# Kernel tuning notes

Measured on AMD Instinct MI355X. Metric: run time of the kernel, lower is better.

The kernel has to match this reference:

```python
import jax, jax.numpy as jnp
import numpy as np

B, S, T = 32, 400, 64
V, E, H = 32000, 256, 512


def _lstm_step(x, h, c, W_ih, W_hh, b):
    # PyTorch LSTM gate order: i, f, g, o
    g = x @ W_ih.T + h @ W_hh.T + b
    i, f, gg, o = jnp.split(g, 4, axis=-1)
    i = jax.nn.sigmoid(i)
    f = jax.nn.sigmoid(f)
    gg = jnp.tanh(gg)
    o = jax.nn.sigmoid(o)
    c_new = f * c + i * gg
    h_new = o * jnp.tanh(c_new)
    return h_new, c_new


def setup_inputs() -> dict:
    key = jax.random.key(0)
    ks = jax.random.split(key, 32)
    d = {}
    d['src'] = jax.random.randint(ks[0], (B, S), 1, V)
    d['src_lengths'] = jnp.full((B,), S, dtype=jnp.int32)
    d['tgt'] = jax.random.randint(ks[1], (B, T), 1, V)
    sc = 0.05
    emb = jax.random.normal(ks[2], (V, E), jnp.float32) * sc
    d['emb'] = emb.at[0].set(0.0)  # padding_idx=0
    d['enc_W_ih_f'] = jax.random.normal(ks[3], (4 * H, E), jnp.float32) * sc
    d['enc_W_hh_f'] = jax.random.normal(ks[4], (4 * H, H), jnp.float32) * sc
    d['enc_b_ih_f'] = jax.random.normal(ks[5], (4 * H,), jnp.float32) * sc
    d['enc_b_hh_f'] = jax.random.normal(ks[6], (4 * H,), jnp.float32) * sc
    d['enc_W_ih_b'] = jax.random.normal(ks[7], (4 * H, E), jnp.float32) * sc
    d['enc_W_hh_b'] = jax.random.normal(ks[8], (4 * H, H), jnp.float32) * sc
    d['enc_b_ih_b'] = jax.random.normal(ks[9], (4 * H,), jnp.float32) * sc
    d['enc_b_hh_b'] = jax.random.normal(ks[10], (4 * H,), jnp.float32) * sc
    d['enc_init_h'] = jax.random.uniform(ks[11], (2, H), jnp.float32, -0.01, 0.01)
    d['enc_init_c'] = jax.random.uniform(ks[12], (2, H), jnp.float32, -0.01, 0.01)
    d['dec_h_W'] = jax.random.normal(ks[13], (H, 2 * H), jnp.float32) * sc
    d['dec_c_W'] = jax.random.normal(ks[14], (H, 2 * H), jnp.float32) * sc
    d['cell_W_ih'] = jax.random.normal(ks[15], (4 * H, E), jnp.float32) * sc
    d['cell_W_hh'] = jax.random.normal(ks[16], (4 * H, H), jnp.float32) * sc
    d['cell_b_ih'] = jax.random.normal(ks[17], (4 * H,), jnp.float32) * sc
    d['cell_b_hh'] = jax.random.normal(ks[18], (4 * H,), jnp.float32) * sc
    d['attn_W'] = jax.random.normal(ks[19], (H, 2 * H), jnp.float32) * sc
    d['attn_b'] = jax.random.normal(ks[20], (H,), jnp.float32) * sc
    d['concat_W'] = jax.random.normal(ks[21], (H, 3 * H), jnp.float32) * sc
    d['concat_b'] = jax.random.normal(ks[22], (H,), jnp.float32) * sc
    d['out_W'] = jax.random.normal(ks[23], (V, H), jnp.float32) * sc
    d['out_b'] = jax.random.normal(ks[24], (V,), jnp.float32) * sc
    return d


def reference(src, src_lengths, tgt, emb,
              enc_W_ih_f, enc_W_hh_f, enc_b_ih_f, enc_b_hh_f,
              enc_W_ih_b, enc_W_hh_b, enc_b_ih_b, enc_b_hh_b,
              enc_init_h, enc_init_c, dec_h_W, dec_c_W,
              cell_W_ih, cell_W_hh, cell_b_ih, cell_b_hh,
              attn_W, attn_b, concat_W, concat_b, out_W, out_b):
    Bs, Ss = src.shape
    Hs = enc_init_h.shape[1]
    xe = emb[src].transpose(1, 0, 2)  # [S, B, E]

    # ---- bi-LSTM encoder (all lengths == S, so packing is identity) ----
    h0f = jnp.broadcast_to(enc_init_h[0], (Bs, Hs))
    c0f = jnp.broadcast_to(enc_init_c[0], (Bs, Hs))
    h0b = jnp.broadcast_to(enc_init_h[1], (Bs, Hs))
    c0b = jnp.broadcast_to(enc_init_c[1], (Bs, Hs))

    def enc_fwd(carry, x):
        h, c = carry
        h, c = _lstm_step(x, h, c, enc_W_ih_f, enc_W_hh_f, enc_b_ih_f + enc_b_hh_f)
        return (h, c), h

    def enc_bwd(carry, x):
        h, c = carry
        h, c = _lstm_step(x, h, c, enc_W_ih_b, enc_W_hh_b, enc_b_ih_b + enc_b_hh_b)
        return (h, c), h

    (hf, cf), out_f = jax.lax.scan(enc_fwd, (h0f, c0f), xe)
    (hb, cb), out_b_seq = jax.lax.scan(enc_bwd, (h0b, c0b), xe[::-1])
    out_b_seq = out_b_seq[::-1]
    enc_outs = jnp.concatenate([out_f, out_b_seq], axis=-1)  # [S, B, 2H]

    # bridge final states to decoder init
    dec_h = jnp.concatenate([hf, hb], axis=-1) @ dec_h_W.T  # [B, H]
    dec_c = jnp.concatenate([cf, cb], axis=-1) @ dec_c_W.T

    mask = jnp.arange(Ss)[None, :] < src_lengths[:, None]  # [B, S]
    attn_keys = enc_outs @ attn_W.T + attn_b  # [S, B, H]

    def dec_step(carry, t_ids):
        h, c = carry
        x = emb[t_ids]  # [B, E]
        h, c = _lstm_step(x, h, c, cell_W_ih, cell_W_hh, cell_b_ih + cell_b_hh)
        scores = jnp.einsum('bh,sbh->bs', h, attn_keys)
        scores = jnp.where(mask, scores, jnp.float32(-1e18))
        w = jax.nn.softmax(scores, axis=1)  # [B, S]
        context = jnp.einsum('bs,sbd->bd', w, enc_outs)  # [B, 2H]
        cc = jnp.tanh(jnp.concatenate([context, h], axis=-1) @ concat_W.T + concat_b)
        logit = jax.nn.log_softmax(cc @ out_W.T + out_b, axis=-1)  # [B, V]
        return (h, c), logit

    _, logits = jax.lax.scan(dec_step, (dec_h, dec_c), tgt.T)  # [T, B, V]
    return logits.transpose(1, 0, 2)  # [B, T, V]
```

## Files before the change

kernel.cpp:

```cpp
#include <hip/hip_runtime.h>
#include <math.h>

#define BB 32
#define SS 400
#define TT 64
#define VV 32000
#define EE 256
#define HH 512

typedef __attribute__((ext_vector_type(4))) float f32x4;
typedef __attribute__((ext_vector_type(8))) short bf16x8t;
typedef __attribute__((ext_vector_type(8))) unsigned short u16x8;
typedef __attribute__((ext_vector_type(4))) unsigned int u32x4;
typedef unsigned long long u64t;

__device__ __forceinline__ ushort f2bf(float x) {
  uint u = __float_as_uint(x);
  return (ushort)((u + 0x7fffu + ((u >> 16) & 1u)) >> 16);
}
__device__ __forceinline__ float bf2f(ushort x) {
  return __uint_as_float(((uint)x) << 16);
}
__device__ __forceinline__ float fsigmoid(float x) {
  return 1.f / (1.f + __expf(-x));
}
__device__ __forceinline__ float ftanh(float x) {
  return 1.f - 2.f / (__expf(2.f * x) + 1.f);
}
__device__ __forceinline__ void gload_lds16(const ushort* g, ushort* l) {
  __builtin_amdgcn_global_load_lds(
      (const __attribute__((address_space(1))) void*)g,
      (__attribute__((address_space(3))) void*)l, 16, 0, 0);
}
__device__ __forceinline__ void unpack8(uint4 u, float* f) {
  f[0] = __uint_as_float(u.x << 16); f[1] = __uint_as_float(u.x & 0xffff0000u);
  f[2] = __uint_as_float(u.y << 16); f[3] = __uint_as_float(u.y & 0xffff0000u);
  f[4] = __uint_as_float(u.z << 16); f[5] = __uint_as_float(u.z & 0xffff0000u);
  f[6] = __uint_as_float(u.w << 16); f[7] = __uint_as_float(u.w & 0xffff0000u);
}

__global__ __launch_bounds__(256) void init_all_kernel(
    const float* __restrict__ einh, uint* __restrict__ hge,
    uint* __restrict__ hgb)
{
  int i = blockIdx.x * 256 + threadIdx.x;
  if (i < 4096) {
    int c = (i & 127) * 4;
    uint lo = (uint)f2bf(einh[c]) | ((uint)f2bf(einh[c + 1]) << 16);
    uint hi = (uint)f2bf(einh[c + 2]) | ((uint)f2bf(einh[c + 3]) << 16);
    u32x4 pkt = {lo, hi, 0u, 0u};
    *(u32x4*)(hge + (size_t)i * 4) = pkt;
  } else if (i < 8192) {
    int p = i - 4096;
    int c = HH + (p & 127) * 4;
    uint lo = (uint)f2bf(einh[c]) | ((uint)f2bf(einh[c + 1]) << 16);
    uint hi = (uint)f2bf(einh[c + 2]) | ((uint)f2bf(einh[c + 3]) << 16);
    u32x4 pkt = {lo, hi, 0u, 0u};
    *(u32x4*)(hgb + (size_t)p * 4) = pkt;
  }
}

__global__ __launch_bounds__(256) void f2bf_kernel(
    const float* __restrict__ in, ushort* __restrict__ out, long n)
{
  long step = (long)gridDim.x * 256 * 4;
  for (long i = ((long)blockIdx.x * 256 + threadIdx.x) * 4; i < n; i += step) {
    float4 v = *(const float4*)(in + i);
    ushort4 o;
    o.x = f2bf(v.x); o.y = f2bf(v.y); o.z = f2bf(v.z); o.w = f2bf(v.w);
    *(ushort4*)(out + i) = o;
  }
}

__global__ __launch_bounds__(64) void gather_x_kernel(
    const float* __restrict__ emb, const int* __restrict__ tok, int L,
    ushort* __restrict__ xout)
{
  int row = blockIdx.x;
  int b = row & 31, s = row >> 5;
  int t = tok[b * L + s];
  float4 v = ((const float4*)(emb + (size_t)t * EE))[threadIdx.x];
  ushort4 o;
  o.x = f2bf(v.x); o.y = f2bf(v.y); o.z = f2bf(v.z); o.w = f2bf(v.w);
  ((ushort4*)(xout + (size_t)row * EE))[threadIdx.x] = o;
}

__global__ __launch_bounds__(256) void bias3_kernel(
    const float* a1, const float* a2, const float* b1, const float* b2,
    const float* c1, const float* c2, float* out)
{
  int i = blockIdx.x * 256 + threadIdx.x;
  if (i < 2048) out[i] = a1[i] + a2[i];
  else if (i < 4096) out[i] = b1[i - 2048] + b2[i - 2048];
  else if (i < 6144) out[i] = c1[i - 4096] + c2[i - 4096];
}

__global__ __launch_bounds__(256) void gemm_mfma_kernel(
    const ushort* __restrict__ A, const ushort* __restrict__ B,
    const float* __restrict__ bias, void* __restrict__ Cout,
    int M, int N, int K, int flags)
{
  __shared__ ushort Asub[128 * 32], Bsub[128 * 32];
  int tid = threadIdx.x;
  int w = tid >> 6, l = tid & 63;
  int n0 = blockIdx.x * 128, m0 = blockIdx.y * 128;
  int wm = w >> 1, wn = w & 1;

  int srow = 16 * 2 * w + (l >> 2);
  int scol = (l & 3) * 8;
  const ushort* Ar0 = A + (size_t)(m0 + srow) * K + scol;
  const ushort* Ar1 = Ar0 + (size_t)16 * K;
  const ushort* Br0 = B + (size_t)(n0 + srow) * K + scol;
  const ushort* Br1 = Br0 + (size_t)16 * K;
  ushort* ldsA0 = Asub + (2 * w) * 512;
  ushort* ldsA1 = Asub + (2 * w + 1) * 512;
  ushort* ldsB0 = Bsub + (2 * w) * 512;
  ushort* ldsB1 = Bsub + (2 * w + 1) * 512;

  f32x4 acc[4][4];
  #pragma unroll
  for (int i = 0; i < 4; ++i)
    #pragma unroll
    for (int j = 0; j < 4; ++j)
      acc[i][j] = (f32x4){0.f, 0.f, 0.f, 0.f};

  int lr = l & 15, lkb = (l >> 4) * 8;

  for (int k0 = 0; k0 < K; k0 += 32) {
    gload_lds16(Ar0 + k0, ldsA0);
    gload_lds16(Ar1 + k0, ldsA1);
    gload_lds16(Br0 + k0, ldsB0);
    gload_lds16(Br1 + k0, ldsB1);
    __syncthreads();
    bf16x8t af[4], bfv[4];
    #pragma unroll
    for (int mf = 0; mf < 4; ++mf)
      af[mf] = *(const bf16x8t*)&Asub[(wm * 64 + mf * 16 + lr) * 32 + lkb];
    #pragma unroll
    for (int nf = 0; nf < 4; ++nf)
      bfv[nf] = *(const bf16x8t*)&Bsub[(wn * 64 + nf * 16 + lr) * 32 + lkb];
    #pragma unroll
    for (int mf = 0; mf < 4; ++mf)
      #pragma unroll
      for (int nf = 0; nf < 4; ++nf)
        acc[mf][nf] = __builtin_amdgcn_mfma_f32_16x16x32_bf16(
            af[mf], bfv[nf], acc[mf][nf], 0, 0, 0);
    __syncthreads();
  }

  int lg = l >> 4;
  #pragma unroll
  for (int mf = 0; mf < 4; ++mf) {
    #pragma unroll
    for (int nf = 0; nf < 4; ++nf) {
      int n = n0 + wn * 64 + nf * 16 + lr;
      float bv = bias[n];
      #pragma unroll
      for (int r = 0; r < 4; ++r) {
        int m = m0 + wm * 64 + mf * 16 + lg * 4 + r;
        float v = acc[mf][nf][r] + bv;
        if (flags & 1) v = tanhf(v);
        if (flags & 8) {
          int s = m >> 5, b = m & 31;
          int gate = n >> 9, col = n & 511;
          size_t dst = (((size_t)s * 32 + (col >> 4)) * 32 + b) * 64 +
                       (size_t)(col & 15) * 4 + gate;
          ((ushort*)Cout)[dst] = f2bf(v);
        } else {
          int row = (flags & 2) ? ((m & 31) * TT + (m >> 5)) : m;
          if (flags & 4) ((ushort*)Cout)[(size_t)row * N + n] = f2bf(v);
          else           ((float*)Cout)[(size_t)row * N + n] = v;
        }
      }
    }
  }
}

struct PersistArgs {
  const float* W_hh;
  const ushort* xw;
  uint* hpack;
  const float* c_init_elem;
  const float* c_init_bcast;
  ushort* out_h;
  int out_os, out_ofs;
  int steps, backward;
  float* h_final;
  float* c_final;
};

__global__ __launch_bounds__(256) void lstm_persist_kernel(
    PersistArgs A0, PersistArgs A1, int nblk_dir,
    const float* __restrict__ cvt_in, ushort* __restrict__ cvt_out, long cvt_n)
{
  __shared__ ushort ldsW[64 * 512];
  __shared__ ushort ldsH[32 * 512];
  __shared__ ushort ldsX[32 * 64];

  int bid = (int)blockIdx.x;
  if (bid >= 2 * nblk_dir) {
    int nc = (int)gridDim.x - 2 * nblk_dir;
    long base = ((long)(bid - 2 * nblk_dir) * 256 + threadIdx.x) * 4;
    long step = (long)nc * 256 * 4;
    for (long i = base; i < cvt_n; i += step) {
      float4 v = *(const float4*)(cvt_in + i);
      ushort4 o;
      o.x = f2bf(v.x); o.y = f2bf(v.y); o.z = f2bf(v.z); o.w = f2bf(v.w);
      *(ushort4*)(cvt_out + i) = o;
    }
    return;
  }

  PersistArgs a = (bid < nblk_dir) ? A0 : A1;
  int cblk = bid % nblk_dir;
  int c0 = cblk * 16;
  int tid = threadIdx.x;
  int w = tid >> 6, l = tid & 63;
  int lr = l & 15, kb = (l >> 4) * 8;
  int g = l & 3;
  int col = c0 + w * 4 + (lr >> 2);
  int n = w * 16 + lr;

  {
    int nn = tid >> 2;
    int kbase = (tid & 3) * 128;
    int rW = (nn & 3) * HH + c0 + (nn >> 2);
    const float4* src = (const float4*)(a.W_hh + (size_t)rW * HH + kbase);
    #pragma unroll
    for (int j = 0; j < 16; ++j) {
      float4 u = src[2 * j], v = src[2 * j + 1];
      u16x8 o;
      o[0] = f2bf(u.x); o[1] = f2bf(u.y); o[2] = f2bf(u.z); o[3] = f2bf(u.w);
      o[4] = f2bf(v.x); o[5] = f2bf(v.y); o[6] = f2bf(v.z); o[7] = f2bf(v.w);
      int k = kbase + j * 8;
      int byte = (nn * 1024 + k * 2) ^ ((nn & 7) << 4);
      *(u16x8*)((char*)ldsW + byte) = o;
    }
  }

  float creg[2][4];
  #pragma unroll
  for (int mf = 0; mf < 2; ++mf)
    #pragma unroll
    for (int r = 0; r < 4; ++r) {
      int b = mf * 16 + (l >> 4) * 4 + r;
      creg[mf][r] = a.c_init_bcast ? a.c_init_bcast[col]
                                   : a.c_init_elem[b * HH + col];
    }
  __syncthreads();

  int prow0 = tid >> 7;
  int pcp4 = tid & 127;

  int s0i = a.backward ? (a.steps - 1) : 0;
  float4 xcur = *(const float4*)(a.xw + ((size_t)s0i * 32 + cblk) * 2048 + tid * 8);
  float4 xnext;

  for (int it = 0; it < a.steps; ++it) {
    int s = a.backward ? (a.steps - 1 - it) : it;
    const uint* hsrc = a.hpack + (size_t)(it & 1) * 4096 * 4;
    uint* hdst = a.hpack + (size_t)((it + 1) & 1) * 4096 * 4;

    u32x4 pv[16];
    #pragma unroll
    for (int j = 0; j < 16; ++j) {
      const uint* ap = hsrc + (size_t)((prow0 + 2 * j) * 128 + pcp4) * 4;
      asm volatile("global_load_dwordx4 %0, %1, off sc0 sc1"
                   : "=&v"(pv[j]) : "v"(ap) : "memory");
    }
    asm volatile("s_waitcnt vmcnt(0)" ::: "memory");
    __builtin_amdgcn_sched_barrier(0);
    {
      int guard = 0;
      while (true) {
        uint bad = 0;
        #pragma unroll
        for (int j = 0; j < 16; ++j) bad |= (pv[j][2] ^ (uint)it);
        if (bad == 0) break;
        if (++guard > (1 << 18)) break;
        __builtin_amdgcn_s_sleep(1);
        #pragma unroll
        for (int j = 0; j < 16; ++j) {
          const uint* ap = hsrc + (size_t)((prow0 + 2 * j) * 128 + pcp4) * 4;
          asm volatile("global_load_dwordx4 %0, %1, off sc0 sc1"
                       : "=&v"(pv[j]) : "v"(ap) : "memory");
        }
        asm volatile("s_waitcnt vmcnt(0)" ::: "memory");
        __builtin_amdgcn_sched_barrier(0);
      }
    }
    __syncthreads();

    #pragma unroll
    for (int j = 0; j < 16; ++j) {
      int row = prow0 + 2 * j;
      int byte = (row * 1024 + pcp4 * 8) ^ ((row & 7) << 4);
      *(u64t*)((char*)ldsH + byte) = ((u64t)pv[j][1] << 32) | (u64t)pv[j][0];
    }
    *(float4*)&ldsX[tid * 8] = xcur;
    __syncthreads();

    f32x4 acc0 = (f32x4){0.f, 0.f, 0.f, 0.f};
    f32x4 acc1 = (f32x4){0.f, 0.f, 0.f, 0.f};
    #pragma unroll
    for (int k0 = 0; k0 < HH; k0 += 32) {
      int ka = k0 + kb;
      bf16x8t av0 = *(const bf16x8t*)((const char*)ldsH + ((lr * 1024 + ka * 2) ^ ((lr & 7) << 4)));
      bf16x8t av1 = *(const bf16x8t*)((const char*)ldsH + (((16 + lr) * 1024 + ka * 2) ^ (((16 + lr) & 7) << 4)));
      int wr = w * 16 + lr;
      bf16x8t bv = *(const bf16x8t*)((const char*)ldsW + ((wr * 1024 + ka * 2) ^ ((wr & 7) << 4)));
      acc0 = __builtin_amdgcn_mfma_f32_16x16x32_bf16(av0, bv, acc0, 0, 0, 0);
      acc1 = __builtin_amdgcn_mfma_f32_16x16x32_bf16(av1, bv, acc1, 0, 0, 0);
    }

    u64t pk[2][4];
    #pragma unroll
    for (int mf = 0; mf < 2; ++mf) {
      f32x4 ac = mf ? acc1 : acc0;
      #pragma unroll
      for (int r = 0; r < 4; ++r) {
        int b = mf * 16 + (l >> 4) * 4 + r;
        float v = ac[r] + bf2f(ldsX[b * 64 + n]);
        float av = (g == 2) ? ftanh(v) : fsigmoid(v);
        float a1 = __shfl_xor(av, 1);
        float a2 = __shfl_xor(av, 2);
        float a3 = __shfl_xor(av, 3);
        float hnew = 0.f;
        if (g == 0) {
          float iv = av, fv = a1, gv = a2, ov = a3;
          float cnew = fv * creg[mf][r] + iv * gv;
          hnew = ov * ftanh(cnew);
          creg[mf][r] = cnew;
          if (a.h_final && it == a.steps - 1) {
            a.h_final[b * HH + col] = hnew;
            a.c_final[b * HH + col] = cnew;
          }
        }
        uint hu = (uint)f2bf(hnew);
        uint p1 = __shfl_xor(hu, 4);
        uint p2 = __shfl_xor(hu, 8);
        uint p3 = __shfl_xor(p1, 8);
        uint lo = hu | (p1 << 16);
        uint hi = p2 | (p3 << 16);
        pk[mf][r] = ((u64t)hi << 32) | (u64t)lo;
      }
    }

    if ((l & 15) == 0 && it + 1 < a.steps) {
      int cp4w = cblk * 4 + w;
      #pragma unroll
      for (int mf = 0; mf < 2; ++mf)
        #pragma unroll
        for (int r = 0; r < 4; ++r) {
          int b = mf * 16 + (l >> 4) * 4 + r;
          u32x4 pkt;
          pkt[0] = (uint)pk[mf][r];
          pkt[1] = (uint)(pk[mf][r] >> 32);
          pkt[2] = (uint)(it + 1);
          pkt[3] = 0u;
          uint* dp = hdst + (size_t)(b * 128 + cp4w) * 4;
          asm volatile("global_store_dwordx4 %0, %1, off sc0 sc1"
                       :: "v"(dp), "v"(pkt) : "memory");
        }
    }

    if ((l & 15) == 0) {
      #pragma unroll
      for (int mf = 0; mf < 2; ++mf)
        #pragma unroll
        for (int r = 0; r < 4; ++r) {
          int b = mf * 16 + (l >> 4) * 4 + r;
          *(u64t*)(a.out_h + (size_t)s * BB * a.out_os + b * a.out_os +
                   a.out_ofs + c0 + w * 4) = pk[mf][r];
        }
    }
    if (it + 1 < a.steps) {
      int sn = a.backward ? (a.steps - 2 - it) : (it + 1);
      const ushort* xp = a.xw + ((size_t)sn * 32 + cblk) * 2048 + tid * 8;
      asm volatile("global_load_dwordx4 %0, %1, off"
                   : "=&v"(xnext) : "v"(xp) : "memory");
    }
    xcur = xnext;
  }
}

__global__ __launch_bounds__(256) void dec_init_kernel(
    const float* __restrict__ hf, const float* __restrict__ hb,
    const float* __restrict__ cf, const float* __restrict__ cb,
    const float* __restrict__ Wh, const float* __restrict__ Wc,
    uint* __restrict__ dh_pack, float* __restrict__ dc)
{
  int b = blockIdx.x;
  __shared__ float hcat[2 * HH], ccat[2 * HH];
  __shared__ ushort dhs[HH];
  int tid = threadIdx.x;
  for (int i = tid; i < HH; i += 256) {
    hcat[i] = hf[b * HH + i]; hcat[HH + i] = hb[b * HH + i];
    ccat[i] = cf[b * HH + i]; ccat[HH + i] = cb[b * HH + i];
  }
  __syncthreads();
  for (int col = tid; col < HH; col += 256) {
    const float4* wh = (const float4*)(Wh + (size_t)col * (2 * HH));
    const float4* wc = (const float4*)(Wc + (size_t)col * (2 * HH));
    float ah = 0.f, acv = 0.f;
    #pragma unroll 4
    for (int k4 = 0; k4 < (2 * HH) / 4; ++k4) {
      float4 h4 = *(const float4*)&hcat[k4 * 4];
      float4 w4 = wh[k4];
      ah += h4.x * w4.x + h4.y * w4.y + h4.z * w4.z + h4.w * w4.w;
      float4 c4 = *(const float4*)&ccat[k4 * 4];
      float4 v4 = wc[k4];
      acv += c4.x * v4.x + c4.y * v4.y + c4.z * v4.z + c4.w * v4.w;
    }
    dhs[col] = f2bf(ah);
    dc[b * HH + col] = acv;
  }
  __syncthreads();
  if (tid < 128) {
    int c = tid * 4;
    uint lo = (uint)dhs[c] | ((uint)dhs[c + 1] << 16);
    uint hi = (uint)dhs[c + 2] | ((uint)dhs[c + 3] << 16);
    u32x4 pkt = {lo, hi, 0u, 0u};
    *(u32x4*)(dh_pack + (size_t)(b * 128 + tid) * 4) = pkt;
  }
}

__global__ __launch_bounds__(256) void scores_kernel(
    const ushort* __restrict__ keys_bf, const ushort* __restrict__ dhall,
    const int* __restrict__ slen, float* __restrict__ sc)
{
  int b = blockIdx.x & 31, s0 = ((int)blockIdx.x >> 5) * 16;
  __shared__ ushort ldsD[64][520];
  __shared__ ushort ldsK[16][520];
  int tid = threadIdx.x;
  #pragma unroll
  for (int j = 0; j < 16; ++j) {
    int ci = tid + 256 * j;
    int row = ci >> 6, c8 = (ci & 63) * 8;
    *(u16x8*)&ldsD[row][c8] = *(const u16x8*)(dhall + ((size_t)row * BB + b) * HH + c8);
  }
  #pragma unroll
  for (int j = 0; j < 4; ++j) {
    int ci = tid + 256 * j;
    int row = ci >> 6, c8 = (ci & 63) * 8;
    *(u16x8*)&ldsK[row][c8] = *(const u16x8*)(keys_bf + ((size_t)(s0 + row) * BB + b) * HH + c8);
  }
  __syncthreads();

  int sl = tid & 15, tq = tid >> 4;
  float acc[4] = {0.f, 0.f, 0.f, 0.f};
  for (int k8 = 0; k8 < 64; ++k8) {
    float kv[8];
    unpack8(*(const uint4*)&ldsK[sl][k8 * 8], kv);
    #pragma unroll
    for (int j = 0; j < 4; ++j) {
      float dv[8];
      unpack8(*(const uint4*)&ldsD[tq * 4 + j][k8 * 8], dv);
      #pragma unroll
      for (int e = 0; e < 8; ++e) acc[j] += kv[e] * dv[e];
    }
  }
  int s = s0 + sl;
  int len = slen[b];
  #pragma unroll
  for (int j = 0; j < 4; ++j) {
    int t = tq * 4 + j;
    sc[((size_t)t * BB + b) * SS + s] = (s < len) ? acc[j] : -1e18f;
  }
}

__global__ __launch_bounds__(64) void softmax_kernel(
    const float* __restrict__ sc, ushort* __restrict__ wbf)
{
  int row = blockIdx.x;
  int tid = threadIdx.x;
  float v[7];
  float m = -3e38f;
  #pragma unroll
  for (int j = 0; j < 7; ++j) {
    int s = tid + 64 * j;
    v[j] = (s < SS) ? sc[(size_t)row * SS + s] : -3e38f;
    m = fmaxf(m, v[j]);
  }
  #pragma unroll
  for (int o = 32; o; o >>= 1) m = fmaxf(m, __shfl_xor(m, o));
  float ssum = 0.f;
  float p[7];
  #pragma unroll
  for (int j = 0; j < 7; ++j) {
    int s = tid + 64 * j;
    p[j] = (s < SS) ? __expf(v[j] - m) : 0.f;
    ssum += p[j];
  }
  #pragma unroll
  for (int o = 32; o; o >>= 1) ssum += __shfl_xor(ssum, o);
  float inv = 1.f / ssum;
  #pragma unroll
  for (int j = 0; j < 7; ++j) {
    int s = tid + 64 * j;
    if (s < 416) wbf[(size_t)row * 416 + s] = (s < SS) ? f2bf(p[j] * inv) : (ushort)0;
  }
}

__global__ __launch_bounds__(256) void context_kernel(
    const ushort* __restrict__ wbf, const ushort* __restrict__ enc,
    const ushort* __restrict__ dhall, ushort* __restrict__ catb)
{
  int b = blockIdx.x, ch = blockIdx.y;
  int tid = threadIdx.x;
  if (ch >= 16) {
    int c0 = (ch - 16) * 64;
    #pragma unroll
    for (int j = 0; j < 2; ++j) {
      int ci = tid + 256 * j;
      int t = ci >> 3, u = ci & 7;
      *(u16x8*)(catb + ((size_t)t * BB + b) * 1536 + 1024 + c0 + u * 8) =
          *(const u16x8*)(dhall + ((size_t)t * BB + b) * HH + c0 + u * 8);
    }
    return;
  }
  int d0 = ch * 64;
  __shared__ ushort ldsWt[64][424];
  for (int ci = tid; ci < 64 * 52; ci += 256) {
    int t = ci / 52, u = ci % 52;
    *(u16x8*)&ldsWt[t][u * 8] = *(const u16x8*)(wbf + (size_t)(t * BB + b) * 416 + u * 8);
  }
  __syncthreads();

  int d = d0 + (tid & 63), tq = tid >> 6;
  float acc16[16];
  #pragma unroll
  for (int i = 0; i < 16; ++i) acc16[i] = 0.f;

  for (int s8 = 0; s8 < 50; ++s8) {
    float ev[8];
    #pragma unroll
    for (int e = 0; e < 8; ++e)
      ev[e] = bf2f(enc[((size_t)(s8 * 8 + e) * BB + b) * 1024 + d]);
    #pragma unroll
    for (int i = 0; i < 16; ++i) {
      float wv[8];
      unpack8(*(const uint4*)&ldsWt[tq * 16 + i][s8 * 8], wv);
      #pragma unroll
      for (int e = 0; e < 8; ++e) acc16[i] += wv[e] * ev[e];
    }
  }
  #pragma unroll
  for (int i = 0; i < 16; ++i) {
    int t = tq * 16 + i;
    catb[((size_t)t * BB + b) * 1536 + d] = f2bf(acc16[i]);
  }
}

__global__ __launch_bounds__(1024) void logsoftmax_kernel(float* __restrict__ out)
{
  int r = blockIdx.x;
  __shared__ float row[VV];
  __shared__ float red[16];
  int tid = threadIdx.x;
  float4* p = (float4*)(out + (size_t)r * VV);
  float4* rp = (float4*)row;
  float m = -3e38f;
  #pragma unroll
  for (int j = 0; j < 8; ++j) {
    int i = tid + 1024 * j;
    if (i < VV / 4) {
      float4 v = p[i];
      rp[i] = v;
      m = fmaxf(m, fmaxf(fmaxf(v.x, v.y), fmaxf(v.z, v.w)));
    }
  }
  #pragma unroll
  for (int o = 32; o; o >>= 1) m = fmaxf(m, __shfl_xor(m, o));
  if ((tid & 63) == 0) red[tid >> 6] = m;
  __syncthreads();
  float mm = red[0];
  #pragma unroll
  for (int i = 1; i < 16; ++i) mm = fmaxf(mm, red[i]);
  __syncthreads();
  float ssum = 0.f;
  #pragma unroll
  for (int j = 0; j < 8; ++j) {
    int i = tid + 1024 * j;
    if (i < VV / 4) {
      float4 v = rp[i];
      ssum += __expf(v.x - mm) + __expf(v.y - mm) + __expf(v.z - mm) + __expf(v.w - mm);
    }
  }
  #pragma unroll
  for (int o = 32; o; o >>= 1) ssum += __shfl_xor(ssum, o);
  if ((tid & 63) == 0) red[tid >> 6] = ssum;
  __syncthreads();
  float st = red[0];
  #pragma unroll
  for (int i = 1; i < 16; ++i) st += red[i];
  st = mm + logf(st);
  #pragma unroll
  for (int j = 0; j < 8; ++j) {
    int i = tid + 1024 * j;
    if (i < VV / 4) {
      float4 v = rp[i];
      v.x -= st; v.y -= st; v.z -= st; v.w -= st;
      p[i] = v;
    }
  }
}

extern "C" void kernel_launch(void* const* d_in, const int* in_sizes, int n_in,
                              void* d_out, int out_size, void* d_ws, size_t ws_size,
                              hipStream_t stream)
{
  (void)in_sizes; (void)n_in; (void)out_size; (void)ws_size;
  const int*   src  = (const int*)d_in[0];
  const int*   slen = (const int*)d_in[1];
  const int*   tgt  = (const int*)d_in[2];
  const float* emb  = (const float*)d_in[3];
  const float* eWif = (const float*)d_in[4];
  const float* eWhf = (const float*)d_in[5];
  const float* ebif = (const float*)d_in[6];
  const float* ebhf = (const float*)d_in[7];
  const float* eWib = (const float*)d_in[8];
  const float* eWhb = (const float*)d_in[9];
  const float* ebib = (const float*)d_in[10];
  const float* ebhb = (const float*)d_in[11];
  const float* einh = (const float*)d_in[12];
  const float* einc = (const float*)d_in[13];
  const float* dhW  = (const float*)d_in[14];
  const float* dcW  = (const float*)d_in[15];
  const float* cWi  = (const float*)d_in[16];
  const float* cWh  = (const float*)d_in[17];
  const float* cbi  = (const float*)d_in[18];
  const float* cbh  = (const float*)d_in[19];
  const float* aW   = (const float*)d_in[20];
  const float* abv  = (const float*)d_in[21];
  const float* ccW  = (const float*)d_in[22];
  const float* ccbv = (const float*)d_in[23];
  const float* oW   = (const float*)d_in[24];
  const float* obv  = (const float*)d_in[25];
  float* out = (float*)d_out;
  float* ws  = (float*)d_ws;

  size_t off = 0;
  ushort* enc_bf  = (ushort*)(ws + off); off += (size_t)SS * BB * 1024 / 2;
  ushort* keys_bf = (ushort*)(ws + off); off += (size_t)SS * BB * HH / 2;
  ushort* dhall_bf= (ushort*)(ws + off); off += (size_t)TT * BB * HH / 2;
  ushort* catb_bf = (ushort*)(ws + off); off += (size_t)TT * BB * 1536 / 2;
  ushort* ccv_bf  = (ushort*)(ws + off); off += (size_t)TT * BB * HH / 2;
  float*  scbuf   = ws + off;            off += (size_t)TT * BB * SS;
  ushort* w_bf    = (ushort*)(ws + off); off += (size_t)TT * BB * 416 / 2;
  ushort* xe_bf   = (ushort*)(ws + off); off += (size_t)SS * BB * EE / 2;
  ushort* xd_bf   = (ushort*)(ws + off); off += (size_t)TT * BB * EE / 2;
  ushort* xWf_bf  = (ushort*)(ws + off); off += (size_t)SS * BB * 2048 / 2;
  ushort* xWb_bf  = (ushort*)(ws + off); off += (size_t)SS * BB * 2048 / 2;
  ushort* xWd_bf  = (ushort*)(ws + off); off += (size_t)TT * BB * 2048 / 2;
  ushort* oW_bf   = (ushort*)(ws + off); off += (size_t)VV * HH / 2;
  ushort* aW_bf   = (ushort*)(ws + off); off += (size_t)HH * 1024 / 2;
  ushort* ccW_bf  = (ushort*)(ws + off); off += (size_t)HH * 1536 / 2;
  ushort* eWif_bf = (ushort*)(ws + off); off += (size_t)2048 * EE / 2;
  ushort* eWib_bf = (ushort*)(ws + off); off += (size_t)2048 * EE / 2;
  ushort* cWi_bf  = (ushort*)(ws + off); off += (size_t)2048 * EE / 2;
  uint* hge_pack = (uint*)(ws + off); off += (size_t)2 * 4096 * 4;
  uint* hgb_pack = (uint*)(ws + off); off += (size_t)2 * 4096 * 4;
  uint* hdec_pack= (uint*)(ws + off); off += (size_t)2 * 4096 * 4;
  float* bias3 = ws + off; off += 3 * 2048;
  float* hf_f  = ws + off; off += BB * HH;
  float* hb_f  = ws + off; off += BB * HH;
  float* cf_f  = ws + off; off += BB * HH;
  float* cb_f  = ws + off; off += BB * HH;
  float* dcb   = ws + off; off += BB * HH;

  hipMemsetAsync(hge_pack, 0, (size_t)3 * 2 * 4096 * 16, stream);

  init_all_kernel<<<64, 256, 0, stream>>>(einh, hge_pack, hgb_pack);

  f2bf_kernel<<<512, 256, 0, stream>>>(aW, aW_bf, (long)HH * 1024);
  f2bf_kernel<<<512, 256, 0, stream>>>(ccW, ccW_bf, (long)HH * 1536);
  f2bf_kernel<<<512, 256, 0, stream>>>(eWif, eWif_bf, (long)2048 * EE);
  f2bf_kernel<<<512, 256, 0, stream>>>(eWib, eWib_bf, (long)2048 * EE);
  f2bf_kernel<<<512, 256, 0, stream>>>(cWi, cWi_bf, (long)2048 * EE);
  bias3_kernel<<<24, 256, 0, stream>>>(ebif, ebhf, ebib, ebhb, cbi, cbh, bias3);

  gather_x_kernel<<<SS * BB, 64, 0, stream>>>(emb, src, SS, xe_bf);
  gather_x_kernel<<<TT * BB, 64, 0, stream>>>(emb, tgt, TT, xd_bf);
  gemm_mfma_kernel<<<dim3(2048 / 128, (SS * BB) / 128), 256, 0, stream>>>(
      xe_bf, eWif_bf, bias3, xWf_bf, SS * BB, 2048, EE, 8);
  gemm_mfma_kernel<<<dim3(2048 / 128, (SS * BB) / 128), 256, 0, stream>>>(
      xe_bf, eWib_bf, bias3 + 2048, xWb_bf, SS * BB, 2048, EE, 8);
  gemm_mfma_kernel<<<dim3(2048 / 128, (TT * BB) / 128), 256, 0, stream>>>(
      xd_bf, cWi_bf, bias3 + 4096, xWd_bf, TT * BB, 2048, EE, 8);

  {
    PersistArgs af, ab;
    af.W_hh = eWhf; af.xw = xWf_bf; af.hpack = hge_pack;
    af.c_init_elem = nullptr; af.c_init_bcast = einc;
    af.out_h = enc_bf; af.out_os = 1024; af.out_ofs = 0;
    af.steps = SS; af.backward = 0;
    af.h_final = hf_f; af.c_final = cf_f;
    ab = af;
    ab.W_hh = eWhb; ab.xw = xWb_bf; ab.hpack = hgb_pack;
    ab.c_init_bcast = einc + HH;
    ab.out_ofs = HH; ab.backward = 1;
    ab.h_final = hb_f; ab.c_final = cb_f;
    lstm_persist_kernel<<<256, 256, 0, stream>>>(af, ab, 32,
                                                 oW, oW_bf, (long)VV * HH);
  }

  dec_init_kernel<<<BB, 256, 0, stream>>>(hf_f, hb_f, cf_f, cb_f, dhW, dcW,
                                          hdec_pack, dcb);
  {
    PersistArgs ad;
    ad.W_hh = cWh; ad.xw = xWd_bf; ad.hpack = hdec_pack;
    ad.c_init_elem = dcb; ad.c_init_bcast = nullptr;
    ad.out_h = dhall_bf; ad.out_os = HH; ad.out_ofs = 0;
    ad.steps = TT; ad.backward = 0;
    ad.h_final = nullptr; ad.c_final = nullptr;
    lstm_persist_kernel<<<32, 256, 0, stream>>>(ad, ad, 32,
                                                nullptr, nullptr, 0);
  }

  gemm_mfma_kernel<<<dim3(HH / 128, (SS * BB) / 128), 256, 0, stream>>>(
      enc_bf, aW_bf, abv, keys_bf, SS * BB, HH, 1024, 4);

  scores_kernel<<<32 * 25, 256, 0, stream>>>(keys_bf, dhall_bf, slen, scbuf);
  softmax_kernel<<<TT * BB, 64, 0, stream>>>(scbuf, w_bf);
  context_kernel<<<dim3(BB, 24), 256, 0, stream>>>(w_bf, enc_bf, dhall_bf, catb_bf);

  gemm_mfma_kernel<<<dim3(HH / 128, (TT * BB) / 128), 256, 0, stream>>>(
      catb_bf, ccW_bf, ccbv, ccv_bf, TT * BB, HH, 1536, 1 | 4);
  gemm_mfma_kernel<<<dim3(VV / 128, (TT * BB) / 128), 256, 0, stream>>>(
      ccv_bf, oW_bf, obv, out, TT * BB, VV, HH, 2);

  logsoftmax_kernel<<<TT * BB, 1024, 0, stream>>>(out);
}
```

Baseline: 3.019 ms.

## Overlap attention-key GEMM and weight conversions with persistent LSTM kernels

```diff
diff --git a/kernel.cpp b/kernel.cpp
--- a/kernel.cpp
+++ b/kernel.cpp
@@ -95,15 +95,14 @@
   else if (i < 6144) out[i] = c1[i - 4096] + c2[i - 4096];
 }
 
-__global__ __launch_bounds__(256) void gemm_mfma_kernel(
+__device__ void gemm_tile_dev(
     const ushort* __restrict__ A, const ushort* __restrict__ B,
     const float* __restrict__ bias, void* __restrict__ Cout,
-    int M, int N, int K, int flags)
-{
-  __shared__ ushort Asub[128 * 32], Bsub[128 * 32];
+    int M, int N, int K, int flags, int m0, int n0,
+    ushort* Asub, ushort* Bsub)
+{
   int tid = threadIdx.x;
   int w = tid >> 6, l = tid & 63;
-  int n0 = blockIdx.x * 128, m0 = blockIdx.y * 128;
   int wm = w >> 1, wn = w & 1;
 
   int srow = 16 * 2 * w + (l >> 2);
@@ -176,6 +175,16 @@
   }
 }
 
+__global__ __launch_bounds__(256) void gemm_mfma_kernel(
+    const ushort* __restrict__ A, const ushort* __restrict__ B,
+    const float* __restrict__ bias, void* __restrict__ Cout,
+    int M, int N, int K, int flags)
+{
+  __shared__ ushort Asub[128 * 32], Bsub[128 * 32];
+  gemm_tile_dev(A, B, bias, Cout, M, N, K, flags,
+                (int)blockIdx.y * 128, (int)blockIdx.x * 128, Asub, Bsub);
+}
+
 struct PersistArgs {
   const float* W_hh;
   const ushort* xw;
@@ -189,24 +198,61 @@
   float* c_final;
 };
 
+struct CvtJobs {
+  const float* in0; ushort* out0; long n0;
+  const float* in1; ushort* out1; long n1;
+  const float* in2; ushort* out2; long n2;
+};
+
+struct AuxGemm {
+  const ushort* A; const ushort* B; const float* bias; void* C;
+  int M, N, K, flags;
+};
+
 __global__ __launch_bounds__(256) void lstm_persist_kernel(
-    PersistArgs A0, PersistArgs A1, int nblk_dir,
-    const float* __restrict__ cvt_in, ushort* __restrict__ cvt_out, long cvt_n)
+    PersistArgs A0, PersistArgs A1, int nblk_dir, int nactive,
+    CvtJobs cv, AuxGemm ag)
 {
   __shared__ ushort ldsW[64 * 512];
   __shared__ ushort ldsH[32 * 512];
   __shared__ ushort ldsX[32 * 64];
 
   int bid = (int)blockIdx.x;
-  if (bid >= 2 * nblk_dir) {
-    int nc = (int)gridDim.x - 2 * nblk_dir;
-    long base = ((long)(bid - 2 * nblk_dir) * 256 + threadIdx.x) * 4;
-    long step = (long)nc * 256 * 4;
-    for (long i = base; i < cvt_n; i += step) {
-      float4 v = *(const float4*)(cvt_in + i);
-      ushort4 o;
-      o.x = f2bf(v.x); o.y = f2bf(v.y); o.z = f2bf(v.z); o.w = f2bf(v.w);
-      *(ushort4*)(cvt_out + i) = o;
+  int tid = threadIdx.x;
+  if (bid >= nactive) {
+    int naux = (int)gridDim.x - nactive;
+    int aid = bid - nactive;
+    if (ag.A) {
+      int nb = ag.N / 128;
+      int ntiles = nb * (ag.M / 128);
+      ushort* Asub = ldsW;
+      ushort* Bsub = ldsW + 128 * 32;
+      for (int t = aid; t < ntiles; t += naux) {
+        gemm_tile_dev(ag.A, ag.B, ag.bias, ag.C, ag.M, ag.N, ag.K, ag.flags,
+                      (t / nb) * 128, (t % nb) * 128, Asub, Bsub);
+        __syncthreads();
+      }
+    } else {
+      long base = ((long)aid * 256 + tid) * 4;
+      long step = (long)naux * 256 * 4;
+      for (long i = base; i < cv.n0; i += step) {
+        float4 v = *(const float4*)(cv.in0 + i);
+        ushort4 o;
+        o.x = f2bf(v.x); o.y = f2bf(v.y); o.z = f2bf(v.z); o.w = f2bf(v.w);
+        *(ushort4*)(cv.out0 + i) = o;
+      }
+      for (long i = base; i < cv.n1; i += step) {
+        float4 v = *(const float4*)(cv.in1 + i);
+        ushort4 o;
+        o.x = f2bf(v.x); o.y = f2bf(v.y); o.z = f2bf(v.z); o.w = f2bf(v.w);
+        *(ushort4*)(cv.out1 + i) = o;
+      }
+      for (long i = base; i < cv.n2; i += step) {
+        float4 v = *(const float4*)(cv.in2 + i);
+        ushort4 o;
+        o.x = f2bf(v.x); o.y = f2bf(v.y); o.z = f2bf(v.z); o.w = f2bf(v.w);
+        *(ushort4*)(cv.out2 + i) = o;
+      }
     }
     return;
   }
@@ -214,7 +260,6 @@
   PersistArgs a = (bid < nblk_dir) ? A0 : A1;
   int cblk = bid % nblk_dir;
   int c0 = cblk * 16;
-  int tid = threadIdx.x;
   int w = tid >> 6, l = tid & 63;
   int lr = l & 15, kb = (l >> 4) * 8;
   int g = l & 3;
@@ -673,8 +718,6 @@
 
   init_all_kernel<<<64, 256, 0, stream>>>(einh, hge_pack, hgb_pack);
 
-  f2bf_kernel<<<512, 256, 0, stream>>>(aW, aW_bf, (long)HH * 1024);
-  f2bf_kernel<<<512, 256, 0, stream>>>(ccW, ccW_bf, (long)HH * 1536);
   f2bf_kernel<<<512, 256, 0, stream>>>(eWif, eWif_bf, (long)2048 * EE);
   f2bf_kernel<<<512, 256, 0, stream>>>(eWib, eWib_bf, (long)2048 * EE);
   f2bf_kernel<<<512, 256, 0, stream>>>(cWi, cWi_bf, (long)2048 * EE);
@@ -701,8 +744,13 @@
     ab.c_init_bcast = einc + HH;
     ab.out_ofs = HH; ab.backward = 1;
     ab.h_final = hb_f; ab.c_final = cb_f;
-    lstm_persist_kernel<<<256, 256, 0, stream>>>(af, ab, 32,
-                                                 oW, oW_bf, (long)VV * HH);
+    CvtJobs cv;
+    cv.in0 = oW;  cv.out0 = oW_bf;  cv.n0 = (long)VV * HH;
+    cv.in1 = aW;  cv.out1 = aW_bf;  cv.n1 = (long)HH * 1024;
+    cv.in2 = ccW; cv.out2 = ccW_bf; cv.n2 = (long)HH * 1536;
+    AuxGemm ag; ag.A = nullptr; ag.B = nullptr; ag.bias = nullptr;
+    ag.C = nullptr; ag.M = 0; ag.N = 0; ag.K = 0; ag.flags = 0;
+    lstm_persist_kernel<<<256, 256, 0, stream>>>(af, ab, 32, 64, cv, ag);
   }
 
   dec_init_kernel<<<BB, 256, 0, stream>>>(hf_f, hb_f, cf_f, cb_f, dhW, dcW,
@@ -714,12 +762,15 @@
     ad.out_h = dhall_bf; ad.out_os = HH; ad.out_ofs = 0;
     ad.steps = TT; ad.backward = 0;
     ad.h_final = nullptr; ad.c_final = nullptr;
-    lstm_persist_kernel<<<32, 256, 0, stream>>>(ad, ad, 32,
-                                                nullptr, nullptr, 0);
-  }
-
-  gemm_mfma_kernel<<<dim3(HH / 128, (SS * BB) / 128), 256, 0, stream>>>(
-      enc_bf, aW_bf, abv, keys_bf, SS * BB, HH, 1024, 4);
+    CvtJobs cv;
+    cv.in0 = nullptr; cv.out0 = nullptr; cv.n0 = 0;
+    cv.in1 = nullptr; cv.out1 = nullptr; cv.n1 = 0;
+    cv.in2 = nullptr; cv.out2 = nullptr; cv.n2 = 0;
+    AuxGemm ag;
+    ag.A = enc_bf; ag.B = aW_bf; ag.bias = abv; ag.C = keys_bf;
+    ag.M = SS * BB; ag.N = HH; ag.K = 1024; ag.flags = 4;
+    lstm_persist_kernel<<<256, 256, 0, stream>>>(ad, ad, 32, 32, cv, ag);
+  }
 
   scores_kernel<<<32 * 25, 256, 0, stream>>>(keys_bf, dhall_bf, slen, scbuf);
   softmax_kernel<<<TT * BB, 64, 0, stream>>>(scbuf, w_bf);
```

After: 3.157 ms. 4.6% more time.
